# Kernel tuning notes

Measured on AMD Instinct MI355X. Metric: run time of the kernel, lower is better.

## Reference

```python
import jax, jax.numpy as jnp
import numpy as np

N = 100000          # active sites
C_IN = 256          # inplanes == outplanes
C_MID = 64          # innerplanes
K = 9               # 3x3 kernel offsets (2D)


def setup_inputs() -> dict:
    key = jax.random.key(0)
    ks = jax.random.split(key, 12)
    features = jax.random.normal(ks[0], (N, C_IN), dtype=jnp.float32)
    # submanifold rulebook: for each active site, index of active neighbor per
    # kernel offset; sentinel N = no active neighbor, center (offset 4) = self
    idx = jax.random.randint(ks[1], (N, K), 0, N, dtype=jnp.int32)
    drop = jax.random.uniform(ks[2], (N, K)) < 0.3
    idx = jnp.where(drop, jnp.int32(N), idx)
    neighbor_idx = idx.at[:, 4].set(jnp.arange(N, dtype=jnp.int32))
    s = 0.05
    return {
        "features": features,
        "neighbor_idx": neighbor_idx,
        "w1": jax.random.normal(ks[3], (C_IN, C_MID), dtype=jnp.float32) * s,
        "scale1": jnp.ones((C_MID,), jnp.float32),
        "bias1": jnp.zeros((C_MID,), jnp.float32),
        "w2": jax.random.normal(ks[4], (K, C_MID, C_MID), dtype=jnp.float32) * s,
        "scale2": jnp.ones((C_MID,), jnp.float32),
        "bias2": jnp.zeros((C_MID,), jnp.float32),
        "w3": jax.random.normal(ks[5], (C_MID, C_IN), dtype=jnp.float32) * s,
        "scale3": jnp.ones((C_IN,), jnp.float32),
        "bias3": jnp.zeros((C_IN,), jnp.float32),
    }


def reference(features, neighbor_idx, w1, scale1, bias1, w2, scale2, bias2,
              w3, scale3, bias3):
    # conv1: 1x1 submanifold conv == per-site matmul; affine BN; ReLU
    out = jax.nn.relu(features @ w1 * scale1 + bias1)            # [N, C_MID]
    # conv2: 3x3 submanifold conv via rulebook gather-matmul-accumulate
    padded = jnp.concatenate([out, jnp.zeros((1, C_MID), out.dtype)], axis=0)
    gathered = padded[neighbor_idx]                               # [N, K, C_MID]
    out = jnp.einsum('nkc,kcd->nd', gathered, w2)                 # [N, C_MID]
    out = jax.nn.relu(out * scale2 + bias2)
    # conv3: 1x1 conv; affine BN; residual add (downsample=None); ReLU
    out = out @ w3 * scale3 + bias3 + features                    # [N, C_IN]
    return jax.nn.relu(out)
```

## Files before the change

### kernel.cpp

```cpp
#include <hip/hip_runtime.h>
#include <stdint.h>

#define C_IN 256
#define C_MID 64
#define KOFF 9

typedef __attribute__((ext_vector_type(8))) short bf16x8;
typedef __attribute__((ext_vector_type(4))) float f32x4;
typedef __attribute__((ext_vector_type(4))) float float4v;

__device__ inline unsigned short f2bf(float f) {
    union { float f; unsigned u; } x; x.f = f;
    unsigned r = x.u + 0x7FFFu + ((x.u >> 16) & 1u);
    return (unsigned short)(r >> 16);
}

__global__ void prep_kernel(const float* __restrict__ w1, const float* __restrict__ s1,
                            const float* __restrict__ w2, const float* __restrict__ s2,
                            const float* __restrict__ w3, const float* __restrict__ s3,
                            unsigned short* __restrict__ w1t,
                            unsigned short* __restrict__ w2t,
                            unsigned short* __restrict__ w3t,
                            unsigned short* __restrict__ zrow) {
    int tid = blockIdx.x * blockDim.x + threadIdx.x;
    int stride = gridDim.x * blockDim.x;
    for (int i = tid; i < C_MID * C_IN; i += stride) {
        int n = i / C_IN, k = i % C_IN;
        w1t[i] = f2bf(w1[k * C_MID + n] * s1[n]);
    }
    for (int i = tid; i < KOFF * C_MID * C_MID; i += stride) {
        int k = i / (C_MID * C_MID);
        int r = i % (C_MID * C_MID);
        int d = r / C_MID, c = r % C_MID;
        w2t[i] = f2bf(w2[(k * C_MID + c) * C_MID + d] * s2[d]);
    }
    for (int i = tid; i < C_IN * C_MID; i += stride) {
        int e = i / C_MID, c = i % C_MID;
        w3t[i] = f2bf(w3[c * C_IN + e] * s3[e]);
    }
    for (int i = tid; i < C_MID; i += stride) zrow[i] = 0;
}

__global__ __launch_bounds__(256, 2) void conv1_kernel(
    const float* __restrict__ feat, const unsigned short* __restrict__ w1t,
    const float* __restrict__ b1, unsigned short* __restrict__ out1, int N)
{
    __shared__ __align__(16) unsigned short sA[64 * 264];
    __shared__ __align__(16) unsigned short sW1[16384];

    int t = threadIdx.x;
    int wave = t >> 6;
    int lane = t & 63;
    int l15 = lane & 15;
    int quad = lane >> 4;
    int row_tile = blockIdx.x * 64;

#pragma unroll
    for (int i = 0; i < 8; ++i) {
        int f = i * 2048 + t * 8;
        int r = f >> 8;
        int c = f & 255;
        int gr = row_tile + r;
        int grc = gr < N ? gr : (N - 1);
        const float4v* p = reinterpret_cast<const float4v*>(feat + (size_t)grc * C_IN + c);
        float4v a0 = p[0];
        float4v a1 = p[1];
        union { unsigned short s[8]; bf16x8 v; } ua;
#pragma unroll
        for (int j = 0; j < 4; ++j) { ua.s[j] = f2bf(a0[j]); ua.s[4 + j] = f2bf(a1[j]); }
        *reinterpret_cast<bf16x8*>(&sA[r * 264 + c]) = ua.v;
    }
    const bf16x8* w1c = reinterpret_cast<const bf16x8*>(w1t);
    bf16x8* sW1c = reinterpret_cast<bf16x8*>(sW1);
#pragma unroll
    for (int it = 0; it < 8; ++it) {
        int s = it * 256 + t;
        int l = s & 15, ct = (s >> 4) & 3, q = (s >> 6) & 3, kk = s >> 8;
        sW1c[s] = w1c[(ct * 16 + l) * 32 + kk * 4 + q];
    }
    __syncthreads();

    float b1v[4];
#pragma unroll
    for (int ct = 0; ct < 4; ++ct) b1v[ct] = b1[ct * 16 + l15];

    int arow = wave * 16 + l15;
    f32x4 acc[4] = {};
#pragma unroll
    for (int kk = 0; kk < 8; ++kk) {
        bf16x8 fa = *reinterpret_cast<const bf16x8*>(&sA[arow * 264 + kk * 32 + quad * 8]);
#pragma unroll
        for (int ct = 0; ct < 4; ++ct) {
            bf16x8 fb = sW1c[((kk * 4 + quad) * 4 + ct) * 16 + l15];
            acc[ct] = __builtin_amdgcn_mfma_f32_16x16x32_bf16(fa, fb, acc[ct], 0, 0, 0);
        }
    }
    int row_base = row_tile + wave * 16;
#pragma unroll
    for (int ct = 0; ct < 4; ++ct) {
#pragma unroll
        for (int reg = 0; reg < 4; ++reg) {
            int row = row_base + quad * 4 + reg;
            if (row < N) {
                float v = acc[ct][reg] + b1v[ct];
                out1[row * C_MID + ct * 16 + l15] = f2bf(fmaxf(v, 0.f));
            }
        }
    }
}

__global__ __launch_bounds__(256, 2) void conv23_kernel(
    const float* __restrict__ feat, const int* __restrict__ nbr,
    const unsigned short* __restrict__ out1, const unsigned short* __restrict__ w2t,
    const float* __restrict__ b2, const unsigned short* __restrict__ w3t,
    const float* __restrict__ b3, float* __restrict__ out, int N)
{
    __shared__ __align__(16) unsigned short sWB[36864];
    __shared__ int sNbr[64 * KOFF];

    int t = threadIdx.x;
    int wave = t >> 6;
    int lane = t & 63;
    int l15 = lane & 15;
    int quad = lane >> 4;
    int row_tile = blockIdx.x * 64;

    bf16x8* sWBc = reinterpret_cast<bf16x8*>(sWB);

    const bf16x8* w2c = reinterpret_cast<const bf16x8*>(w2t);
#pragma unroll
    for (int it = 0; it < 18; ++it) {
        int s = it * 256 + t;
        int l = s & 15, ct = (s >> 4) & 3, q = (s >> 6) & 3, kk = (s >> 8) & 1, k = s >> 9;
        sWBc[s] = w2c[k * 512 + (ct * 16 + l) * 8 + kk * 4 + q];
    }
#pragma unroll
    for (int i = 0; i < 3; ++i) {
        int j = i * 256 + t;
        if (j < 64 * KOFF) {
            int g = row_tile * KOFF + j;
            sNbr[j] = (g < N * KOFF) ? nbr[g] : N;
        }
    }
    __syncthreads();

    int rt = wave * 16 + l15;
    int nb[KOFF];
#pragma unroll
    for (int k = 0; k < KOFF; ++k) nb[k] = sNbr[rt * KOFF + k];

    bf16x8 ga[KOFF][2];
#pragma unroll
    for (int k = 0; k < KOFF; ++k) {
        const bf16x8* pg = reinterpret_cast<const bf16x8*>(out1 + (size_t)nb[k] * C_MID + quad * 8);
        ga[k][0] = pg[0];
        ga[k][1] = pg[4];
    }
    __builtin_amdgcn_sched_barrier(0);

    f32x4 acc2[4] = {};
#pragma unroll
    for (int k = 0; k < KOFF; ++k) {
#pragma unroll
        for (int kk = 0; kk < 2; ++kk) {
#pragma unroll
            for (int ct = 0; ct < 4; ++ct) {
                bf16x8 fb = sWBc[((k * 2 + kk) * 4 + quad) * 64 + ct * 16 + l15];
                acc2[ct] = __builtin_amdgcn_mfma_f32_16x16x32_bf16(ga[k][kk], fb, acc2[ct], 0, 0, 0);
            }
        }
    }
    __syncthreads();

    unsigned short* mid = &sWB[32256];
#pragma unroll
    for (int ct = 0; ct < 4; ++ct) {
        float bb = b2[ct * 16 + l15];
#pragma unroll
        for (int reg = 0; reg < 4; ++reg) {
            float v = fmaxf(acc2[ct][reg] + bb, 0.f);
            mid[(wave * 16 + quad * 4 + reg) * 72 + ct * 16 + l15] = f2bf(v);
        }
    }
    const bf16x8* w3c = reinterpret_cast<const bf16x8*>(w3t);
#pragma unroll
    for (int it = 0; it < 8; ++it) {
        int s = it * 256 + t;
        int l = s & 15, c2 = (s >> 4) & 15, q = (s >> 8) & 3, kk = (s >> 10) & 1;
        sWBc[s] = w3c[(c2 * 16 + l) * 8 + kk * 4 + q];
    }
    __syncthreads();

    f32x4 acc3[16] = {};
#pragma unroll
    for (int kk = 0; kk < 2; ++kk) {
        bf16x8 fa = *reinterpret_cast<const bf16x8*>(
            &mid[(wave * 16 + l15) * 72 + kk * 32 + quad * 8]);
#pragma unroll
        for (int c2 = 0; c2 < 16; ++c2) {
            bf16x8 fb = sWBc[((kk * 4 + quad) * 16 + c2) * 16 + l15];
            acc3[c2] = __builtin_amdgcn_mfma_f32_16x16x32_bf16(fa, fb, acc3[c2], 0, 0, 0);
        }
    }
    int row_base = row_tile + wave * 16;
#pragma unroll
    for (int c2 = 0; c2 < 16; ++c2) {
        float bb = b3[c2 * 16 + l15];
#pragma unroll
        for (int reg = 0; reg < 4; ++reg) {
            int row = row_base + quad * 4 + reg;
            if (row < N) {
                int o = row * C_IN + c2 * 16 + l15;
                float v = acc3[c2][reg] + bb + feat[o];
                out[o] = fmaxf(v, 0.f);
            }
        }
    }
}

extern "C" void kernel_launch(void* const* d_in, const int* in_sizes, int n_in,
                              void* d_out, int out_size, void* d_ws, size_t ws_size,
                              hipStream_t stream) {
    const float* feat = (const float*)d_in[0];
    const int*   nbr  = (const int*)d_in[1];
    const float* w1   = (const float*)d_in[2];
    const float* s1   = (const float*)d_in[3];
    const float* b1   = (const float*)d_in[4];
    const float* w2   = (const float*)d_in[5];
    const float* s2   = (const float*)d_in[6];
    const float* b2   = (const float*)d_in[7];
    const float* w3   = (const float*)d_in[8];
    const float* s3   = (const float*)d_in[9];
    const float* b3   = (const float*)d_in[10];
    float* out = (float*)d_out;
    int N = in_sizes[0] / C_IN;

    char* ws = (char*)d_ws;
    unsigned short* w1t  = (unsigned short*)(ws);
    unsigned short* w2t  = (unsigned short*)(ws + 32768);
    unsigned short* w3t  = (unsigned short*)(ws + 32768 + 73728);
    unsigned short* out1 = (unsigned short*)(ws + 139264);

    prep_kernel<<<80, 256, 0, stream>>>(w1, s1, w2, s2, w3, s3, w1t, w2t, w3t,
                                        out1 + (size_t)N * C_MID);
    int nblk = (N + 63) / 64;
    conv1_kernel<<<nblk, 256, 0, stream>>>(feat, w1t, b1, out1, N);
    conv23_kernel<<<nblk, 256, 0, stream>>>(feat, nbr, out1, w2t, b2, w3t, b3, out, N);
}
```

Before: 310.9 us.

## Transpose MFMA operands so each lane owns a site row, enabling vector loads/stores

Swaps the A/B operands of every MFMA so the accumulator layout gives each lane four consecutive output channels for one site. conv1 now loads its features straight from global memory into registers and converts them there, which removes the shared staging tile and lets the launch bound ask for more blocks per CU. conv23 prefetches the residual features early alongside the neighbour gather, and all epilogues use vectorized float4/short4 stores instead of scalar strided ones. In exchange, conv1 uses more registers, and the residual prefetch adds register pressure in conv23.

```diff
diff --git a/kernel.cpp b/kernel.cpp
--- a/kernel.cpp
+++ b/kernel.cpp
@@ -6,6 +6,7 @@
 #define KOFF 9
 
 typedef __attribute__((ext_vector_type(8))) short bf16x8;
+typedef __attribute__((ext_vector_type(4))) short short4v;
 typedef __attribute__((ext_vector_type(4))) float f32x4;
 typedef __attribute__((ext_vector_type(4))) float float4v;
 
@@ -41,11 +42,10 @@
     for (int i = tid; i < C_MID; i += stride) zrow[i] = 0;
 }
 
-__global__ __launch_bounds__(256, 2) void conv1_kernel(
+__global__ __launch_bounds__(256, 4) void conv1_kernel(
     const float* __restrict__ feat, const unsigned short* __restrict__ w1t,
     const float* __restrict__ b1, unsigned short* __restrict__ out1, int N)
 {
-    __shared__ __align__(16) unsigned short sA[64 * 264];
     __shared__ __align__(16) unsigned short sW1[16384];
 
     int t = threadIdx.x;
@@ -54,22 +54,9 @@
     int l15 = lane & 15;
     int quad = lane >> 4;
     int row_tile = blockIdx.x * 64;
-
-#pragma unroll
-    for (int i = 0; i < 8; ++i) {
-        int f = i * 2048 + t * 8;
-        int r = f >> 8;
-        int c = f & 255;
-        int gr = row_tile + r;
-        int grc = gr < N ? gr : (N - 1);
-        const float4v* p = reinterpret_cast<const float4v*>(feat + (size_t)grc * C_IN + c);
-        float4v a0 = p[0];
-        float4v a1 = p[1];
-        union { unsigned short s[8]; bf16x8 v; } ua;
-#pragma unroll
-        for (int j = 0; j < 4; ++j) { ua.s[j] = f2bf(a0[j]); ua.s[4 + j] = f2bf(a1[j]); }
-        *reinterpret_cast<bf16x8*>(&sA[r * 264 + c]) = ua.v;
-    }
+    int site = row_tile + wave * 16 + l15;
+    int sitec = site < N ? site : (N - 1);
+
     const bf16x8* w1c = reinterpret_cast<const bf16x8*>(w1t);
     bf16x8* sW1c = reinterpret_cast<bf16x8*>(sW1);
 #pragma unroll
@@ -78,33 +65,43 @@
         int l = s & 15, ct = (s >> 4) & 3, q = (s >> 6) & 3, kk = s >> 8;
         sW1c[s] = w1c[(ct * 16 + l) * 32 + kk * 4 + q];
     }
-    __syncthreads();
-
-    float b1v[4];
-#pragma unroll
-    for (int ct = 0; ct < 4; ++ct) b1v[ct] = b1[ct * 16 + l15];
-
-    int arow = wave * 16 + l15;
+
+    float4v fr[16];
+#pragma unroll
+    for (int kk = 0; kk < 8; ++kk) {
+        const float4v* p = reinterpret_cast<const float4v*>(
+            feat + (size_t)sitec * C_IN + kk * 32 + quad * 8);
+        fr[kk * 2] = p[0];
+        fr[kk * 2 + 1] = p[1];
+    }
+    __builtin_amdgcn_sched_barrier(0);
+    __syncthreads();
+
     f32x4 acc[4] = {};
 #pragma unroll
     for (int kk = 0; kk < 8; ++kk) {
-        bf16x8 fa = *reinterpret_cast<const bf16x8*>(&sA[arow * 264 + kk * 32 + quad * 8]);
+        union { unsigned short s[8]; bf16x8 v; } ua;
+#pragma unroll
+        for (int j = 0; j < 4; ++j) {
+            ua.s[j] = f2bf(fr[kk * 2][j]);
+            ua.s[4 + j] = f2bf(fr[kk * 2 + 1][j]);
+        }
 #pragma unroll
         for (int ct = 0; ct < 4; ++ct) {
-            bf16x8 fb = sW1c[((kk * 4 + quad) * 4 + ct) * 16 + l15];
-            acc[ct] = __builtin_amdgcn_mfma_f32_16x16x32_bf16(fa, fb, acc[ct], 0, 0, 0);
-        }
-    }
-    int row_base = row_tile + wave * 16;
-#pragma unroll
-    for (int ct = 0; ct < 4; ++ct) {
-#pragma unroll
-        for (int reg = 0; reg < 4; ++reg) {
-            int row = row_base + quad * 4 + reg;
-            if (row < N) {
-                float v = acc[ct][reg] + b1v[ct];
-                out1[row * C_MID + ct * 16 + l15] = f2bf(fmaxf(v, 0.f));
-            }
+            bf16x8 fa = sW1c[((kk * 4 + quad) * 4 + ct) * 16 + l15];
+            acc[ct] = __builtin_amdgcn_mfma_f32_16x16x32_bf16(fa, ua.v, acc[ct], 0, 0, 0);
+        }
+    }
+    if (site < N) {
+#pragma unroll
+        for (int ct = 0; ct < 4; ++ct) {
+            const float4v* bp = reinterpret_cast<const float4v*>(b1 + ct * 16 + quad * 4);
+            float4v bb = bp[0];
+            union { unsigned short s[4]; short4v v; } o;
+#pragma unroll
+            for (int reg = 0; reg < 4; ++reg)
+                o.s[reg] = f2bf(fmaxf(acc[ct][reg] + bb[reg], 0.f));
+            *reinterpret_cast<short4v*>(out1 + (size_t)site * C_MID + ct * 16 + quad * 4) = o.v;
         }
     }
 }
@@ -124,6 +121,8 @@
     int l15 = lane & 15;
     int quad = lane >> 4;
     int row_tile = blockIdx.x * 64;
+    int site = row_tile + wave * 16 + l15;
+    int sitec = site < N ? site : (N - 1);
 
     bf16x8* sWBc = reinterpret_cast<bf16x8*>(sWB);
 
@@ -156,6 +155,11 @@
         ga[k][0] = pg[0];
         ga[k][1] = pg[4];
     }
+    float4v rf[16];
+#pragma unroll
+    for (int c2 = 0; c2 < 16; ++c2)
+        rf[c2] = *reinterpret_cast<const float4v*>(
+            feat + (size_t)sitec * C_IN + c2 * 16 + quad * 4);
     __builtin_amdgcn_sched_barrier(0);
 
     f32x4 acc2[4] = {};
@@ -165,22 +169,23 @@
         for (int kk = 0; kk < 2; ++kk) {
 #pragma unroll
             for (int ct = 0; ct < 4; ++ct) {
-                bf16x8 fb = sWBc[((k * 2 + kk) * 4 + quad) * 64 + ct * 16 + l15];
-                acc2[ct] = __builtin_amdgcn_mfma_f32_16x16x32_bf16(ga[k][kk], fb, acc2[ct], 0, 0, 0);
+                bf16x8 fa = sWBc[((k * 2 + kk) * 4 + quad) * 64 + ct * 16 + l15];
+                acc2[ct] = __builtin_amdgcn_mfma_f32_16x16x32_bf16(fa, ga[k][kk], acc2[ct], 0, 0, 0);
             }
         }
     }
     __syncthreads();
 
-    unsigned short* mid = &sWB[32256];
+    unsigned short* mid = &sWB[31744];
 #pragma unroll
     for (int ct = 0; ct < 4; ++ct) {
-        float bb = b2[ct * 16 + l15];
-#pragma unroll
-        for (int reg = 0; reg < 4; ++reg) {
-            float v = fmaxf(acc2[ct][reg] + bb, 0.f);
-            mid[(wave * 16 + quad * 4 + reg) * 72 + ct * 16 + l15] = f2bf(v);
-        }
+        const float4v* bp = reinterpret_cast<const float4v*>(b2 + ct * 16 + quad * 4);
+        float4v bb = bp[0];
+        union { unsigned short s[4]; short4v v; } o;
+#pragma unroll
+        for (int reg = 0; reg < 4; ++reg)
+            o.s[reg] = f2bf(fmaxf(acc2[ct][reg] + bb[reg], 0.f));
+        *reinterpret_cast<short4v*>(&mid[(wave * 16 + l15) * 80 + ct * 16 + quad * 4]) = o.v;
     }
     const bf16x8* w3c = reinterpret_cast<const bf16x8*>(w3t);
 #pragma unroll
@@ -194,26 +199,24 @@
     f32x4 acc3[16] = {};
 #pragma unroll
     for (int kk = 0; kk < 2; ++kk) {
-        bf16x8 fa = *reinterpret_cast<const bf16x8*>(
-            &mid[(wave * 16 + l15) * 72 + kk * 32 + quad * 8]);
+        bf16x8 fb = *reinterpret_cast<const bf16x8*>(
+            &mid[(wave * 16 + l15) * 80 + kk * 32 + quad * 8]);
 #pragma unroll
         for (int c2 = 0; c2 < 16; ++c2) {
-            bf16x8 fb = sWBc[((kk * 4 + quad) * 16 + c2) * 16 + l15];
+            bf16x8 fa = sWBc[((kk * 4 + quad) * 16 + c2) * 16 + l15];
             acc3[c2] = __builtin_amdgcn_mfma_f32_16x16x32_bf16(fa, fb, acc3[c2], 0, 0, 0);
         }
     }
-    int row_base = row_tile + wave * 16;
-#pragma unroll
-    for (int c2 = 0; c2 < 16; ++c2) {
-        float bb = b3[c2 * 16 + l15];
-#pragma unroll
-        for (int reg = 0; reg < 4; ++reg) {
-            int row = row_base + quad * 4 + reg;
-            if (row < N) {
-                int o = row * C_IN + c2 * 16 + l15;
-                float v = acc3[c2][reg] + bb + feat[o];
-                out[o] = fmaxf(v, 0.f);
-            }
+    if (site < N) {
+#pragma unroll
+        for (int c2 = 0; c2 < 16; ++c2) {
+            const float4v* bp = reinterpret_cast<const float4v*>(b3 + c2 * 16 + quad * 4);
+            float4v bb = bp[0];
+            float4v o;
+#pragma unroll
+            for (int reg = 0; reg < 4; ++reg)
+                o[reg] = fmaxf(acc3[c2][reg] + bb[reg] + rf[c2][reg], 0.f);
+            *reinterpret_cast<float4v*>(out + (size_t)site * C_IN + c2 * 16 + quad * 4) = o;
         }
     }
 }
```

Result: faster. 263.8 us (-15.1%).
